# Kernel tuning notes

Hardware: AMD Instinct MI355X
Metric: run time of the kernel (lower is better)

## Reference

```python
import jax, jax.numpy as jnp
import numpy as np

DIM = 192; HEADS = 6; WS = 8; OVERLAP = 2; PAD = 3; STRIDE = WS - OVERLAP; HID = DIM * 4

_coords = np.stack(np.meshgrid(np.arange(WS), np.arange(WS), indexing='ij'), 0).reshape(2, -1)
_rel = (_coords[:, :, None] - _coords[:, None, :]).transpose(1, 2, 0).astype(np.int64)
_rel[..., 0] += WS - 1; _rel[..., 1] += WS - 1; _rel[..., 0] *= 2 * WS - 1
REL_IDX = jnp.asarray(_rel.sum(-1).reshape(-1))  # (WS^2 * WS^2,)


def _ln_c(x, g, b):
    # LayerNorm over channel dim of NCHW (LayerNormProxy)
    mu = jnp.mean(x, axis=1, keepdims=True)
    var = jnp.mean((x - mu) ** 2, axis=1, keepdims=True)
    return (x - mu) * jax.lax.rsqrt(var + 1e-5) * g[:, None, None] + b[:, None, None]


def _conv1x1(x, w, b):
    return jnp.einsum('bchw,oc->bohw', x, w) + b[:, None, None]


def _dwconv3(x, w, b):
    y = jax.lax.conv_general_dilated(x, w, (1, 1), ((1, 1), (1, 1)),
                                     feature_group_count=x.shape[1],
                                     dimension_numbers=('NCHW', 'OIHW', 'NCHW'))
    return y + b[:, None, None]


def _unfold(x, k, s, p):
    # F.unfold: (B,C,H,W) -> (B, C*k*k, L) with (C,kh,kw) channel order, row-major windows
    B, C, H, W = x.shape
    xp = jnp.pad(x, ((0, 0), (0, 0), (p, p), (p, p)))
    Lh = (H + 2 * p - k) // s + 1; Lw = (W + 2 * p - k) // s + 1
    ih = (jnp.arange(Lh) * s)[:, None] + jnp.arange(k)  # (Lh,k)
    iw = (jnp.arange(Lw) * s)[:, None] + jnp.arange(k)  # (Lw,k)
    t = xp[:, :, ih, :][:, :, :, :, iw]                 # (B,C,Lh,k,Lw,k)
    t = t.transpose(0, 1, 3, 5, 2, 4)                   # (B,C,k,k,Lh,Lw)
    return t.reshape(B, C * k * k, Lh * Lw)


def _fold(cols, h, w, k, s, p):
    # F.fold: (B, C*k*k, L) -> (B,C,h,w), summing overlaps
    B = cols.shape[0]
    Lh = (h + 2 * p - k) // s + 1; Lw = (w + 2 * p - k) // s + 1
    C = cols.shape[1] // (k * k)
    t = cols.reshape(B, C, k, k, Lh, Lw).transpose(0, 1, 4, 2, 5, 3)  # (B,C,Lh,k,Lw,k)
    ih = (jnp.arange(Lh) * s)[:, None] + jnp.arange(k)
    iw = (jnp.arange(Lw) * s)[:, None] + jnp.arange(k)
    out = jnp.zeros((B, C, h + 2 * p, w + 2 * p), cols.dtype)
    out = out.at[:, :, ih[:, :, None, None], iw[None, None, :, :]].add(t)
    return out[:, :, p:p + h, p:p + w]


def _reverse(win, h, w):
    B, L, nH, ws2, ch = win.shape
    cols = win.transpose(0, 2, 4, 3, 1).reshape(B, nH * ch * ws2, L)
    return _fold(cols, h, w, WS, STRIDE, PAD)


def _hft(x, w, b):
    # HFTAttention: high-frequency residual of multi-scale avg pools, dw-conv sigmoid gate
    B, C, h, ww = x.shape
    a = 3.0 * x
    for s in (2, 4, 8):
        pool = x.reshape(B, C, h // s, s, ww // s, s).mean(axis=(3, 5))
        a = a - jnp.repeat(jnp.repeat(pool, s, axis=2), s, axis=3)
    return jax.nn.sigmoid(_dwconv3(a, w, b)) * x


def _forward(x, n1g, n1b, qkv_w, qkv_b, temp, rpb, proj_w, proj_b, hft_w, hft_b,
             n2g, n2b, fc1_w, fc1_b, sgn_g, sgn_b, sg_w, sg_b, fc2_w, fc2_b):
    B, C, H, W = x.shape
    ch = C // HEADS
    y = _conv1x1(_ln_c(x, n1g, n1b), qkv_w, qkv_b)       # (B,3C,H,W)
    cols = _unfold(y, WS, STRIDE, PAD)
    L = cols.shape[-1]
    win = cols.reshape(B, 3 * HEADS, ch, WS * WS, L).transpose(0, 4, 1, 3, 2)  # (B,L,3H,ws2,ch)
    q = win[:, :, :HEADS] * temp[None, None]
    k = win[:, :, HEADS:2 * HEADS]
    v = win[:, :, 2 * HEADS:]
    attn = jnp.einsum('blhic,blhjc->blhij', q, k)
    bias = rpb[REL_IDX].reshape(WS * WS, WS * WS, HEADS).transpose(2, 0, 1)
    attn = attn + bias[None, None]
    e = jnp.exp(attn - jnp.max(attn, axis=-1, keepdims=True))
    s = jnp.sum(e, axis=-1, keepdims=True)               # (B,L,H,ws2,1)
    s_img = _reverse(s, H, W)                            # (B,HEADS,H,W): folded softmax denom
    o = jnp.einsum('blhij,blhjc->blhic', e, v)
    o_img = _reverse(o, H, W).reshape(B, HEADS, ch, H, W)
    out = (o_img / s_img[:, :, None]).reshape(B, C, H, W)
    out = _hft(_conv1x1(out, proj_w, proj_b), hft_w, hft_b)
    x1 = x + out
    z = jax.nn.gelu(_conv1x1(_ln_c(x1, n2g, n2b), fc1_w, fc1_b), approximate=False)
    z1, z2 = jnp.split(z, 2, axis=1)
    z = z1 * _dwconv3(_ln_c(z2, sgn_g, sgn_b), sg_w, sg_b)
    return x1 + _conv1x1(z, fc2_w, fc2_b)


def setup_inputs() -> dict:
    key = jax.random.key(0)
    ks = jax.random.split(key, 8)
    B, Hi, Wi = 4, 128, 128
    f = jnp.float32
    return {
        'x': jax.random.normal(ks[0], (B, DIM, Hi, Wi), f),
        'n1g': jnp.ones((DIM,), f), 'n1b': jnp.zeros((DIM,), f),
        'qkv_w': jax.random.normal(ks[1], (3 * DIM, DIM), f) * 0.02,
        'qkv_b': jnp.zeros((3 * DIM,), f),
        'temp': jnp.ones((HEADS, 1, 1), f),
        'rpb': jax.random.normal(ks[2], ((2 * WS - 1) ** 2, HEADS), f) * 0.02,
        'proj_w': jax.random.normal(ks[3], (DIM, DIM), f) * 0.02,
        'proj_b': jnp.zeros((DIM,), f),
        'hft_w': jax.random.normal(ks[4], (DIM, 1, 3, 3), f) * 0.02,
        'hft_b': jnp.zeros((DIM,), f),
        'n2g': jnp.ones((DIM,), f), 'n2b': jnp.zeros((DIM,), f),
        'fc1_w': jax.random.normal(ks[5], (HID, DIM), f) * 0.02,
        'fc1_b': jnp.zeros((HID,), f),
        'sgn_g': jnp.ones((HID // 2,), f), 'sgn_b': jnp.zeros((HID // 2,), f),
        'sg_w': jax.random.normal(ks[6], (HID // 2, 1, 3, 3), f) * 0.02,
        'sg_b': jnp.zeros((HID // 2,), f),
        'fc2_w': jax.random.normal(ks[7], (DIM, HID // 2), f) * 0.02,
        'fc2_b': jnp.zeros((DIM,), f),
    }


def reference(x, n1g, n1b, qkv_w, qkv_b, temp, rpb, proj_w, proj_b, hft_w, hft_b,
              n2g, n2b, fc1_w, fc1_b, sgn_g, sgn_b, sg_w, sg_b, fc2_w, fc2_b):
    return _forward(x, n1g, n1b, qkv_w, qkv_b, temp, rpb, proj_w, proj_b, hft_w, hft_b,
                    n2g, n2b, fc1_w, fc1_b, sgn_g, sgn_b, sg_w, sg_b, fc2_w, fc2_b)
```

## Files before the change

### kernel.cpp

```cpp
#include <hip/hip_runtime.h>
#include <math.h>

static constexpr int B_    = 4;
static constexpr int C_    = 192;
static constexpr int NPIX  = 16384;
static constexpr int PTOT  = B_ * NPIX;
static constexpr int HEADS = 6;
static constexpr int STR   = 6;
static constexpr int LH    = 22;
static constexpr int LWIN  = LH * LH;
static constexpr int NWIN  = B_ * LWIN;

typedef short bf16x8 __attribute__((ext_vector_type(8)));
typedef float f32x4  __attribute__((ext_vector_type(4)));

__device__ __forceinline__ unsigned short f2bf(float f) {
    union { float f; unsigned int u; } v; v.f = f;
    return (unsigned short)((v.u + 0x8000u) >> 16);
}
__device__ __forceinline__ float bf2f(unsigned short h) {
    union { unsigned int u; float f; } v; v.u = ((unsigned int)h) << 16;
    return v.f;
}
__device__ __forceinline__ float gelu_f(float v) {
    float u2 = 2.f * v * (0.7978845608f + 0.0356774081f * v * v);
    float e = __expf(u2);
    float th = 1.f - 2.f / (e + 1.f);
    return 0.5f * v * (1.f + th);
}

__global__ __launch_bounds__(256) void prep_k(const float* __restrict__ W, const float* __restrict__ g,
                                              const float* __restrict__ bln, const float* __restrict__ bias,
                                              int M, int K,
                                              unsigned short* __restrict__ wgb, float* __restrict__ wsum,
                                              float* __restrict__ wb) {
    int o = blockIdx.x * 256 + threadIdx.x;
    if (o >= M) return;
    float sum = 0.f, bb = 0.f;
    for (int c = 0; c < K; ++c) {
        float wv = W[(size_t)o * K + c];
        float wgv = wv * g[c];
        wgb[(size_t)o * K + c] = f2bf(wgv);
        sum += wgv;
        bb += wv * bln[c];
    }
    wsum[o] = sum;
    wb[o] = bb + bias[o];
}

__global__ __launch_bounds__(256) void wcvt_k(const float* __restrict__ W, unsigned short* __restrict__ Wb, int n) {
    int i = blockIdx.x * 256 + threadIdx.x;
    if (i < n) Wb[i] = f2bf(W[i]);
}

template <typename T, bool LNS>
__global__ __launch_bounds__(256) void transpose_k(const T* __restrict__ in, unsigned short* __restrict__ out,
                                                   int Cn, int bstride, float2* __restrict__ ps) {
    __shared__ float tile[64][65];
    int n0 = blockIdx.x << 6, c0 = blockIdx.y << 6, b = blockIdx.z;
    int t = threadIdx.x, r = t >> 2, cg = (t & 3) << 4;
    const T* ib = in + (size_t)b * bstride;
    if constexpr (sizeof(T) == 4) {
        const float4* src = (const float4*)(ib + (size_t)(c0 + r) * NPIX + n0 + cg);
        #pragma unroll
        for (int j = 0; j < 4; ++j) {
            float4 v = src[j];
            tile[r][cg + 4 * j + 0] = v.x; tile[r][cg + 4 * j + 1] = v.y;
            tile[r][cg + 4 * j + 2] = v.z; tile[r][cg + 4 * j + 3] = v.w;
        }
    } else {
        const uint4* src = (const uint4*)((const unsigned short*)ib + (size_t)(c0 + r) * NPIX + n0 + cg);
        uint4 v0 = src[0], v1 = src[1];
        unsigned int arr[8] = {v0.x, v0.y, v0.z, v0.w, v1.x, v1.y, v1.z, v1.w};
        #pragma unroll
        for (int j = 0; j < 8; ++j) {
            tile[r][cg + 2 * j]     = bf2f((unsigned short)(arr[j] & 0xFFFFu));
            tile[r][cg + 2 * j + 1] = bf2f((unsigned short)(arr[j] >> 16));
        }
    }
    __syncthreads();
    unsigned int pk[8];
    float s = 0.f, s2 = 0.f;
    #pragma unroll
    for (int j = 0; j < 8; ++j) {
        float a  = tile[cg + 2 * j][r];
        float c2 = tile[cg + 2 * j + 1][r];
        if (LNS) { s += a + c2; s2 += a * a + c2 * c2; }
        pk[j] = (unsigned int)f2bf(a) | ((unsigned int)f2bf(c2) << 16);
    }
    uint4* dst = (uint4*)(out + ((size_t)(b << 14) + n0 + r) * Cn + c0 + cg);
    dst[0] = make_uint4(pk[0], pk[1], pk[2], pk[3]);
    dst[1] = make_uint4(pk[4], pk[5], pk[6], pk[7]);
    if (LNS) {
        s  += __shfl_xor(s, 1);  s  += __shfl_xor(s, 2);
        s2 += __shfl_xor(s2, 1); s2 += __shfl_xor(s2, 2);
        if ((t & 3) == 0)
            ps[((b * gridDim.y + blockIdx.y) << 14) + n0 + r] = make_float2(s, s2);
    }
}

__global__ __launch_bounds__(256) void lnfin_k(const float2* __restrict__ ps, int nch, float invC,
                                               float* __restrict__ mu, float* __restrict__ rs) {
    int p = blockIdx.x * 256 + threadIdx.x;
    int b = p >> 14, n = p & (NPIX - 1);
    float s = 0.f, s2 = 0.f;
    for (int c = 0; c < nch; ++c) {
        float2 v = ps[((b * nch + c) << 14) + n];
        s += v.x; s2 += v.y;
    }
    float m = s * invC;
    mu[p] = m;
    rs[p] = rsqrtf(s2 * invC - m * m + 1e-5f);
}

template <int KK, int ACT, bool LN, bool RES, bool OBF, int STATS>
__global__ __launch_bounds__(256) void gemm2_k(const unsigned short* __restrict__ Wb,
                                               const unsigned short* __restrict__ Xt,
                                               void* __restrict__ outv,
                                               const float* __restrict__ mu, const float* __restrict__ rs,
                                               const float* __restrict__ wsum, const float* __restrict__ wb,
                                               const float* __restrict__ resid, int M,
                                               float* __restrict__ smu, float* __restrict__ srs) {
    constexpr int LDK    = KK + 8;
    constexpr int KSTEPS = KK / 32;
    __shared__ unsigned short xs[64 * LDK];

    int t = threadIdx.x;
    int pt = blockIdx.x;
    int b  = pt >> 8;
    int n0 = (pt & 255) << 6;

    const unsigned short* xg = Xt + (size_t)(b * NPIX + n0) * KK;
    constexpr int NJ = KK / 8;
    #pragma unroll
    for (int i = 0; i < 64 * NJ / 256; ++i) {
        int c = i * 256 + t;
        int p, j;
        if (KK == 192) { p = (c * 2731) >> 16; j = c - p * 24; }
        else           { int q = c >> 4; p = (q * 21846) >> 16; j = c - p * 48; }
        uint4 v = *(const uint4*)(xg + (size_t)c * 8);
        *(uint4*)&xs[p * LDK + j * 8] = v;
    }
    __syncthreads();

    int w  = t >> 6, l = t & 63;
    int wr = w >> 1, wc = w & 1;
    int lr = l & 15, kb = l >> 4;
    int pw = wr * 32;

    bf16x8 afr[KSTEPS][2];
    #pragma unroll
    for (int ks = 0; ks < KSTEPS; ++ks)
        #pragma unroll
        for (int m = 0; m < 2; ++m)
            afr[ks][m] = *(const bf16x8*)&xs[(pw + m * 16 + lr) * LDK + ks * 32 + kb * 8];

    float muv[2][4], rsv[2][4], murs[2][4];
    if (LN) {
        #pragma unroll
        for (int m = 0; m < 2; ++m) {
            int nidx = n0 + pw + m * 16 + kb * 4;
            #pragma unroll
            for (int r = 0; r < 4; ++r) {
                muv[m][r] = mu[(b << 14) + nidx + r];
                rsv[m][r] = rs[(b << 14) + nidx + r];
                murs[m][r] = muv[m][r] * rsv[m][r];
            }
        }
    }

    float zs[2][4], zs2[2][4];
    bool dstats = STATS && (blockIdx.y == gridDim.y - 1);
    if (STATS) {
        #pragma unroll
        for (int m = 0; m < 2; ++m)
            #pragma unroll
            for (int r = 0; r < 4; ++r) { zs[m][r] = 0.f; zs2[m][r] = 0.f; }
    }

    int mpb = (M >> 6) / gridDim.y;
    int ocbase = blockIdx.y * mpb;
    #pragma unroll 2
    for (int oc = 0; oc < mpb; ++oc) {
        int ow = ((ocbase + oc) << 6) + wc * 32;
        f32x4 acc[2][2];
        #pragma unroll
        for (int m = 0; m < 2; ++m)
            #pragma unroll
            for (int n = 0; n < 2; ++n) acc[m][n] = (f32x4){0.f, 0.f, 0.f, 0.f};

        #pragma unroll
        for (int ks = 0; ks < KSTEPS; ++ks) {
            bf16x8 bfr[2];
            #pragma unroll
            for (int n = 0; n < 2; ++n)
                bfr[n] = *(const bf16x8*)(Wb + (size_t)(ow + n * 16 + lr) * KK + ks * 32 + kb * 8);
            #pragma unroll
            for (int m = 0; m < 2; ++m)
                #pragma unroll
                for (int n = 0; n < 2; ++n)
                    acc[m][n] = __builtin_amdgcn_mfma_f32_16x16x32_bf16(afr[ks][m], bfr[n], acc[m][n], 0, 0, 0);
        }

        #pragma unroll
        for (int m = 0; m < 2; ++m) {
            int nidx = n0 + pw + m * 16 + kb * 4;
            #pragma unroll
            for (int n = 0; n < 2; ++n) {
                int o = ow + n * 16 + lr;
                float wbv = wb[o];
                float wsv = 0.f; if (LN) wsv = wsum[o];
                size_t obase = (((size_t)b * M + o) << 14) + nidx;
                float rv[4] = {0.f, 0.f, 0.f, 0.f};
                if (RES) {
                    float4 rr = *(const float4*)(resid + obase);
                    rv[0] = rr.x; rv[1] = rr.y; rv[2] = rr.z; rv[3] = rr.w;
                }
                float vo[4];
                #pragma unroll
                for (int r = 0; r < 4; ++r) {
                    float a = acc[m][n][r];
                    float v;
                    if (LN) { float t1 = fmaf(-murs[m][r], wsv, wbv); v = fmaf(rsv[m][r], a, t1); }
                    else    v = a + wbv;
                    if (ACT == 1) v = gelu_f(v);
                    vo[r] = v + rv[r];
                    if (STATS) {
                        if (dstats) { zs[m][r] += vo[r]; zs2[m][r] += vo[r] * vo[r]; }
                    }
                }
                if (OBF) {
                    ushort4 u;
                    u.x = f2bf(vo[0]); u.y = f2bf(vo[1]); u.z = f2bf(vo[2]); u.w = f2bf(vo[3]);
                    *(ushort4*)((unsigned short*)outv + obase) = u;
                } else {
                    float4 f = {vo[0], vo[1], vo[2], vo[3]};
                    *(float4*)((float*)outv + obase) = f;
                }
            }
        }
    }

    if (STATS) {
        if (dstats) {
            __shared__ float sst[64][2][2];
            #pragma unroll
            for (int m = 0; m < 2; ++m)
                #pragma unroll
                for (int r = 0; r < 4; ++r) {
                    float a  = zs[m][r], c2 = zs2[m][r];
                    a  += __shfl_xor(a, 1);  a  += __shfl_xor(a, 2);  a  += __shfl_xor(a, 4);  a  += __shfl_xor(a, 8);
                    c2 += __shfl_xor(c2, 1); c2 += __shfl_xor(c2, 2); c2 += __shfl_xor(c2, 4); c2 += __shfl_xor(c2, 8);
                    if (lr == 0) {
                        int pp = pw + m * 16 + kb * 4 + r;
                        sst[pp][wc][0] = a; sst[pp][wc][1] = c2;
                    }
                }
            __syncthreads();
            if (t < 64) {
                float ss  = sst[t][0][0] + sst[t][1][0];
                float ss2 = sst[t][0][1] + sst[t][1][1];
                float invC = 1.f / (float)(mpb << 6);
                float mm = ss * invC;
                smu[(b << 14) + n0 + t] = mm;
                srs[(b << 14) + n0 + t] = rsqrtf(ss2 * invC - mm * mm + 1e-5f);
            }
        }
    }
}

__global__ __launch_bounds__(64) void attn_mfma_k(const unsigned short* __restrict__ qkv,
                                                  const float* __restrict__ rpb,
                                                  const float* __restrict__ temp,
                                                  unsigned short* __restrict__ o_win,
                                                  float* __restrict__ s_win) {
    __shared__ unsigned short p_lds[64 * 72];
    __shared__ float rp[225];
    int wh = blockIdx.x;
    int head = wh % HEADS;
    int bw = wh / HEADS;
    int b = bw / LWIN, l = bw % LWIN;
    int sh = l / LH, sw = l % LH;
    int h0 = sh * STR - 3, w0 = sw * STR - 3;
    int t = threadIdx.x;
    int lr = t & 15, kb = t >> 4;

    for (int i = t; i < 225; i += 64) rp[i] = rpb[i * HEADS + head];
    float tmp = temp[head];

    const size_t qbase = ((size_t)(b * 576 + head * 32)) << 14;
    const unsigned short* qp = qkv + qbase;
    const unsigned short* kp = qkv + qbase + ((size_t)192 << 14);
    const unsigned short* vp = qkv + qbase + ((size_t)384 << 14);

    bf16x8 kf[4], qf[4];
    #pragma unroll
    for (int m = 0; m < 4; ++m) {
        int jp = m * 16 + lr;
        int hh = h0 + (jp >> 3), ww = w0 + (jp & 7);
        bool ok = ((unsigned)hh < 128u) && ((unsigned)ww < 128u);
        int pix = (hh << 7) + ww;
        #pragma unroll
        for (int j = 0; j < 8; ++j) {
            unsigned short kv = 0, qv = 0;
            if (ok) {
                size_t off = ((size_t)(kb * 8 + j) << 14) + pix;
                kv = kp[off];
                qv = qp[off];
            }
            kf[m][j] = (short)kv;
            qf[m][j] = (short)qv;
        }
    }

    f32x4 st[4][4];
    #pragma unroll
    for (int m = 0; m < 4; ++m)
        #pragma unroll
        for (int n = 0; n < 4; ++n) st[m][n] = (f32x4){0.f, 0.f, 0.f, 0.f};
    #pragma unroll
    for (int m = 0; m < 4; ++m)
        #pragma unroll
        for (int n = 0; n < 4; ++n)
            st[m][n] = __builtin_amdgcn_mfma_f32_16x16x32_bf16(kf[m], qf[n], st[m][n], 0, 0, 0);

    bf16x8 vf[2][2];
    #pragma unroll
    for (int np = 0; np < 2; ++np) {
        #pragma unroll
        for (int ks = 0; ks < 2; ++ks) {
            int hh = h0 + ks * 4 + kb;
            bool okr = (unsigned)hh < 128u;
            const unsigned short* vrow = vp + (((size_t)(np * 16 + lr)) << 14) + (hh << 7) + w0;
            #pragma unroll
            for (int j = 0; j < 8; ++j) {
                int ww = w0 + j;
                unsigned short vv = 0;
                if (okr && (unsigned)ww < 128u) vv = vrow[j];
                vf[np][ks][j] = (short)vv;
            }
        }
    }

    __syncthreads();

    #pragma unroll
    for (int n = 0; n < 4; ++n) {
        int i = n * 16 + lr;
        int iyy = i >> 3, ixx = i & 7;
        #pragma unroll
        for (int m = 0; m < 4; ++m) {
            #pragma unroll
            for (int r = 0; r < 4; ++r) {
                int j = m * 16 + kb * 4 + r;
                int dy = iyy - (j >> 3) + 7;
                int dx = ixx - (j & 7) + 7;
                st[m][n][r] = st[m][n][r] * tmp + rp[dy * 15 + dx];
            }
        }
    }

    #pragma unroll
    for (int n = 0; n < 4; ++n) {
        float mx = -1e30f;
        #pragma unroll
        for (int m = 0; m < 4; ++m)
            #pragma unroll
            for (int r = 0; r < 4; ++r) mx = fmaxf(mx, st[m][n][r]);
        mx = fmaxf(mx, __shfl_xor(mx, 16));
        mx = fmaxf(mx, __shfl_xor(mx, 32));
        float s = 0.f;
        #pragma unroll
        for (int m = 0; m < 4; ++m) {
            #pragma unroll
            for (int r = 0; r < 4; ++r) {
                float e = __expf(st[m][n][r] - mx);
                st[m][n][r] = e;
                s += e;
            }
        }
        s += __shfl_xor(s, 16);
        s += __shfl_xor(s, 32);
        int i = n * 16 + lr;
        if (kb == 0) s_win[(size_t)wh * 64 + i] = s;
        #pragma unroll
        for (int m = 0; m < 4; ++m) {
            unsigned int lo = (unsigned int)f2bf(st[m][n][0]) | ((unsigned int)f2bf(st[m][n][1]) << 16);
            unsigned int hi = (unsigned int)f2bf(st[m][n][2]) | ((unsigned int)f2bf(st[m][n][3]) << 16);
            *(unsigned int*)&p_lds[i * 72 + m * 16 + kb * 4]     = lo;
            *(unsigned int*)&p_lds[i * 72 + m * 16 + kb * 4 + 2] = hi;
        }
    }

    __syncthreads();

    f32x4 oc[4][2];
    #pragma unroll
    for (int m = 0; m < 4; ++m)
        #pragma unroll
        for (int np = 0; np < 2; ++np) oc[m][np] = (f32x4){0.f, 0.f, 0.f, 0.f};
    #pragma unroll
    for (int ks = 0; ks < 2; ++ks) {
        bf16x8 pa[4];
        #pragma unroll
        for (int m = 0; m < 4; ++m)
            pa[m] = *(const bf16x8*)&p_lds[(m * 16 + lr) * 72 + ks * 32 + kb * 8];
        #pragma unroll
        for (int m = 0; m < 4; ++m)
            #pragma unroll
            for (int np = 0; np < 2; ++np)
                oc[m][np] = __builtin_amdgcn_mfma_f32_16x16x32_bf16(pa[m], vf[np][ks], oc[m][np], 0, 0, 0);
    }

    unsigned short* ob = o_win + (size_t)wh * 2048;
    #pragma unroll
    for (int m = 0; m < 4; ++m) {
        int ibase = m * 16 + kb * 4;
        #pragma unroll
        for (int np = 0; np < 2; ++np) {
            int c = np * 16 + lr;
            #pragma unroll
            for (int r = 0; r < 4; ++r)
                ob[(ibase + r) * 32 + c] = f2bf(oc[m][np][r]);
        }
    }
}

__device__ __forceinline__ void win_range(int h, int& s0, int& s1) {
    s0 = (h + 1) / 6; if (s0 < 0) s0 = 0;
    s1 = (h + 3) / 6; if (s1 > 21) s1 = 21;
}

__global__ __launch_bounds__(256) void simg_k(const float* __restrict__ s_win, float* __restrict__ s_img) {
    int tid = blockIdx.x * 256 + threadIdx.x;
    if (tid >= B_ * HEADS * NPIX) return;
    int n = tid & (NPIX - 1);
    int bh = tid >> 14;
    int hd = bh % HEADS, b = bh / HEADS;
    int hy = n >> 7, wx = n & 127;
    int sy0, sy1, sx0, sx1;
    win_range(hy, sy0, sy1);
    win_range(wx, sx0, sx1);
    float acc = 0.f;
    for (int sy = sy0; sy <= sy1; ++sy)
        for (int sx = sx0; sx <= sx1; ++sx) {
            int idx = (hy - (sy * 6 - 3)) * 8 + (wx - (sx * 6 - 3));
            acc += s_win[(size_t)((b * LWIN + sy * LH + sx) * HEADS + hd) * 64 + idx];
        }
    s_img[tid] = acc;
}

__global__ __launch_bounds__(256) void fold_k(const unsigned short* __restrict__ o_win,
                                              const float* __restrict__ s_img,
                                              unsigned short* __restrict__ attn_t) {
    int tid = blockIdx.x * 256 + threadIdx.x;
    int q = (int)((((unsigned long long)(tid >> 3)) * 174763ull) >> 19);
    int oct = tid - q * 24;
    int n = q & (NPIX - 1), b = q >> 14;
    int hd = oct >> 2, c8 = (oct & 3) << 3;
    int hy = n >> 7, wx = n & 127;
    int sy0, sy1, sx0, sx1;
    win_range(hy, sy0, sy1);
    win_range(wx, sx0, sx1);
    float acc[8] = {0.f, 0.f, 0.f, 0.f, 0.f, 0.f, 0.f, 0.f};
    for (int sy = sy0; sy <= sy1; ++sy)
        for (int sx = sx0; sx <= sx1; ++sx) {
            int idx = (hy - (sy * 6 - 3)) * 8 + (wx - (sx * 6 - 3));
            const unsigned short* p = o_win + ((size_t)((b * LWIN + sy * LH + sx) * HEADS + hd) * 2048 + idx * 32 + c8);
            uint4 v = *(const uint4*)p;
            unsigned int arr[4] = {v.x, v.y, v.z, v.w};
            #pragma unroll
            for (int j = 0; j < 4; ++j) {
                acc[2 * j]     += bf2f((unsigned short)(arr[j] & 0xFFFFu));
                acc[2 * j + 1] += bf2f((unsigned short)(arr[j] >> 16));
            }
        }
    float inv = 1.f / s_img[((b * HEADS + hd) << 14) + n];
    unsigned int pk[4];
    #pragma unroll
    for (int j = 0; j < 4; ++j) {
        unsigned int lo = f2bf(acc[2 * j] * inv);
        unsigned int hi = f2bf(acc[2 * j + 1] * inv);
        pk[j] = lo | (hi << 16);
    }
    *(uint4*)&attn_t[((size_t)((b << 14) + n)) * 192 + hd * 32 + c8] = make_uint4(pk[0], pk[1], pk[2], pk[3]);
}

__global__ __launch_bounds__(256) void halve_k(const float* __restrict__ in, float* __restrict__ out, int Win) {
    int Wo = Win >> 1;
    int tot = B_ * C_ * Wo * Wo;
    int tid = blockIdx.x * 256 + threadIdx.x;
    if (tid >= tot) return;
    int xy = tid % (Wo * Wo);
    int bc = tid / (Wo * Wo);
    int y = xy / Wo, x = xy % Wo;
    const float* p = in + (size_t)bc * Win * Win + (size_t)(2 * y) * Win + 2 * x;
    out[tid] = 0.25f * (p[0] + p[1] + p[Win] + p[Win + 1]);
}

__global__ __launch_bounds__(256) void hft_fused_k(const float* __restrict__ po, const float* __restrict__ x,
                                                   const float* __restrict__ p2, const float* __restrict__ p4,
                                                   const float* __restrict__ p8, const float* __restrict__ hw,
                                                   const float* __restrict__ hb, float* __restrict__ x1) {
    __shared__ float tile[34 * 133];
    int rt = blockIdx.x, ch = blockIdx.y, b = blockIdx.z;
    int bc = b * C_ + ch;
    int y0 = rt << 5;
    int t = threadIdx.x;
    const float* pob = po + ((size_t)bc << 14);
    const float* p2b = p2 + ((size_t)bc << 12);
    const float* p4b = p4 + ((size_t)bc << 10);
    const float* p8b = p8 + ((size_t)bc << 8);

    for (int idx = t; idx < 34 * 133; idx += 256) {
        int row = idx / 133, col = idx - row * 133;
        int yy = y0 + row - 1, xw = col - 1;
        float val = 0.f;
        if (col < 130 && (unsigned)yy < 128u && (unsigned)xw < 128u) {
            int nn = (yy << 7) + xw;
            val = 3.f * pob[nn]
                - p2b[((yy >> 1) << 6) + (xw >> 1)]
                - p4b[((yy >> 2) << 5) + (xw >> 2)]
                - p8b[((yy >> 3) << 4) + (xw >> 3)];
        }
        tile[idx] = val;
    }
    __syncthreads();

    float wv[9];
    #pragma unroll
    for (int k = 0; k < 9; ++k) wv[k] = hw[ch * 9 + k];
    float hbv = hb[ch];

    int r = t & 31, c0 = (t >> 5) << 4;
    int nbase = ((y0 + r) << 7) + c0;
    const float* xb = x + ((size_t)bc << 14);
    float* x1b = x1 + ((size_t)bc << 14);

    float pov[16], xv[16];
    #pragma unroll
    for (int j4 = 0; j4 < 4; ++j4) {
        float4 pp = *(const float4*)(pob + nbase + 4 * j4);
        float4 xx = *(const float4*)(xb + nbase + 4 * j4);
        pov[4*j4] = pp.x; pov[4*j4+1] = pp.y; pov[4*j4+2] = pp.z; pov[4*j4+3] = pp.w;
        xv[4*j4] = xx.x;  xv[4*j4+1] = xx.y;  xv[4*j4+2] = xx.z;  xv[4*j4+3] = xx.w;
    }
    float res[16];
    #pragma unroll
    for (int j = 0; j < 16; ++j) {
        float acc = hbv;
        #pragma unroll
        for (int dy = 0; dy < 3; ++dy)
            #pragma unroll
            for (int dx = 0; dx < 3; ++dx)
                acc += wv[dy * 3 + dx] * tile[(r + dy) * 133 + c0 + j + dx];
        float sg = 1.f / (1.f + __expf(-acc));
        res[j] = xv[j] + sg * pov[j];
    }
    #pragma unroll
    for (int j4 = 0; j4 < 4; ++j4) {
        float4 o = {res[4*j4], res[4*j4+1], res[4*j4+2], res[4*j4+3]};
        *(float4*)(x1b + nbase + 4 * j4) = o;
    }
}

__global__ __launch_bounds__(256) void sgmul_k(unsigned short* __restrict__ z,
                                               const float* __restrict__ mu3, const float* __restrict__ rs3,
                                               const float* __restrict__ sgn_g, const float* __restrict__ sgn_b,
                                               const float* __restrict__ sg_w, const float* __restrict__ sg_b) {
    __shared__ float tile[34 * 133];
    int rt = blockIdx.x, ch = blockIdx.y, b = blockIdx.z;
    int y0 = rt << 5;
    int t = threadIdx.x;
    const unsigned short* zb = z + ((size_t)(b * 768 + 384 + ch) << 14);
    unsigned short* z1p = z + ((size_t)(b * 768 + ch) << 14);
    const float* mub = mu3 + (b << 14);
    const float* rsb = rs3 + (b << 14);
    float g = sgn_g[ch], bb = sgn_b[ch];

    for (int idx = t; idx < 34 * 133; idx += 256) {
        int row = idx / 133, col = idx - row * 133;
        int yy = y0 + row - 1, xw = col - 1;
        float val = 0.f;
        if (col < 130 && (unsigned)yy < 128u && (unsigned)xw < 128u) {
            int nn = (yy << 7) + xw;
            val = (bf2f(zb[nn]) - mub[nn]) * rsb[nn] * g + bb;
        }
        tile[idx] = val;
    }
    __syncthreads();

    float wv[9];
    #pragma unroll
    for (int k = 0; k < 9; ++k) wv[k] = sg_w[ch * 9 + k];
    float sb = sg_b[ch];

    int r = t & 31, c0 = (t >> 5) << 4;
    int nbase = ((y0 + r) << 7) + c0;

    float res[16];
    #pragma unroll
    for (int j = 0; j < 16; ++j) {
        float acc = sb;
        #pragma unroll
        for (int dy = 0; dy < 3; ++dy)
            #pragma unroll
            for (int dx = 0; dx < 3; ++dx)
                acc += wv[dy * 3 + dx] * tile[(r + dy) * 133 + c0 + j + dx];
        res[j] = acc;
    }
    uint4* zp = (uint4*)(z1p + nbase);
    uint4 v0 = zp[0], v1 = zp[1];
    unsigned int arr[8] = {v0.x, v0.y, v0.z, v0.w, v1.x, v1.y, v1.z, v1.w};
    #pragma unroll
    for (int j = 0; j < 8; ++j) {
        float lo = bf2f((unsigned short)(arr[j] & 0xFFFFu)) * res[2 * j];
        float hi = bf2f((unsigned short)(arr[j] >> 16)) * res[2 * j + 1];
        arr[j] = (unsigned int)f2bf(lo) | ((unsigned int)f2bf(hi) << 16);
    }
    zp[0] = make_uint4(arr[0], arr[1], arr[2], arr[3]);
    zp[1] = make_uint4(arr[4], arr[5], arr[6], arr[7]);
}

extern "C" void kernel_launch(void* const* d_in, const int* in_sizes, int n_in,
                              void* d_out, int out_size, void* d_ws, size_t ws_size,
                              hipStream_t stream) {
    const float* x     = (const float*)d_in[0];
    const float* n1g   = (const float*)d_in[1];
    const float* n1b   = (const float*)d_in[2];
    const float* qkv_w = (const float*)d_in[3];
    const float* qkv_b = (const float*)d_in[4];
    const float* temp  = (const float*)d_in[5];
    const float* rpb   = (const float*)d_in[6];
    const float* proj_w= (const float*)d_in[7];
    const float* proj_b= (const float*)d_in[8];
    const float* hft_w = (const float*)d_in[9];
    const float* hft_b = (const float*)d_in[10];
    const float* n2g   = (const float*)d_in[11];
    const float* n2b   = (const float*)d_in[12];
    const float* fc1_w = (const float*)d_in[13];
    const float* fc1_b = (const float*)d_in[14];
    const float* sgn_g = (const float*)d_in[15];
    const float* sgn_b = (const float*)d_in[16];
    const float* sg_w  = (const float*)d_in[17];
    const float* sg_b  = (const float*)d_in[18];
    const float* fc2_w = (const float*)d_in[19];
    const float* fc2_b = (const float*)d_in[20];
    float* out = (float*)d_out;
    float* w = (float*)d_ws;

    float* mu1 = w;            float* rs1 = w + 65536;
    float* mu2 = w + 131072;   float* rs2 = w + 196608;
    float* mu3 = w + 262144;   float* rs3 = w + 327680;
    unsigned short* wgb_qkv = (unsigned short*)(w + 393216);
    float* wsum_qkv = w + 448512;  float* wb_qkv = w + 449088;
    unsigned short* wgb_fc1 = (unsigned short*)(w + 449664);
    float* wsum_fc1 = w + 523392;  float* wb_fc1 = w + 524160;
    unsigned short* pwb  = (unsigned short*)(w + 524928);
    unsigned short* f2wb = (unsigned short*)(w + 543360);
    unsigned short* xt     = (unsigned short*)(w + 580224);
    unsigned short* attn_t = xt;
    unsigned short* qkvb = (unsigned short*)(w + 6871680);
    float* proj_out = w + 6871680;
    float* p2 = w + 19454592;  float* p4 = w + 22600320;  float* p8 = w + 23386752;
    unsigned short* x1t  = (unsigned short*)(w + 6871680);
    unsigned short* z1t  = (unsigned short*)(w + 6871680);
    unsigned short* o_win = (unsigned short*)(w + 25746048);
    float* s_win = w + 49535616;
    float* s_img = w + 50279040;
    unsigned short* z = (unsigned short*)(w + 25746048);
    float* x1 = w + 50911872;
    float2* ps = (float2*)(w + 19454592);

    transpose_k<float, true><<<dim3(256, 3, B_), 256, 0, stream>>>(x, xt, 192, 192 * NPIX, ps);
    lnfin_k<<<256, 256, 0, stream>>>(ps, 3, 1.f / 192.f, mu1, rs1);
    prep_k<<<3, 256, 0, stream>>>(qkv_w, n1g, n1b, qkv_b, 576, 192, wgb_qkv, wsum_qkv, wb_qkv);
    gemm2_k<192, 0, true, false, true, 0><<<dim3(1024, 3), 256, 0, stream>>>(
        wgb_qkv, xt, qkvb, mu1, rs1, wsum_qkv, wb_qkv, nullptr, 576, nullptr, nullptr);
    attn_mfma_k<<<NWIN * HEADS, 64, 0, stream>>>(qkvb, rpb, temp, o_win, s_win);
    simg_k<<<1536, 256, 0, stream>>>(s_win, s_img);
    fold_k<<<6144, 256, 0, stream>>>(o_win, s_img, attn_t);
    wcvt_k<<<144, 256, 0, stream>>>(proj_w, pwb, 192 * 192);
    gemm2_k<192, 0, false, false, false, 0><<<dim3(1024, 3), 256, 0, stream>>>(
        pwb, attn_t, proj_out, nullptr, nullptr, nullptr, proj_b, nullptr, 192, nullptr, nullptr);
    halve_k<<<12288, 256, 0, stream>>>(proj_out, p2, 128);
    halve_k<<<3072, 256, 0, stream>>>(p2, p4, 64);
    halve_k<<<768, 256, 0, stream>>>(p4, p8, 32);
    hft_fused_k<<<dim3(4, 192, B_), 256, 0, stream>>>(proj_out, x, p2, p4, p8, hft_w, hft_b, x1);
    transpose_k<float, true><<<dim3(256, 3, B_), 256, 0, stream>>>(x1, x1t, 192, 192 * NPIX, ps);
    lnfin_k<<<256, 256, 0, stream>>>(ps, 3, 1.f / 192.f, mu2, rs2);
    prep_k<<<3, 256, 0, stream>>>(fc1_w, n2g, n2b, fc1_b, 768, 192, wgb_fc1, wsum_fc1, wb_fc1);
    gemm2_k<192, 1, true, false, true, 1><<<dim3(1024, 2), 256, 0, stream>>>(
        wgb_fc1, x1t, z, mu2, rs2, wsum_fc1, wb_fc1, nullptr, 768, mu3, rs3);
    sgmul_k<<<dim3(4, 384, B_), 256, 0, stream>>>(z, mu3, rs3, sgn_g, sgn_b, sg_w, sg_b);
    transpose_k<unsigned short, false><<<dim3(256, 6, B_), 256, 0, stream>>>(z, z1t, 384, 768 * NPIX, nullptr);
    wcvt_k<<<288, 256, 0, stream>>>(fc2_w, f2wb, 192 * 384);
    gemm2_k<384, 0, false, true, false, 0><<<dim3(1024, 1), 256, 0, stream>>>(
        f2wb, z1t, out, nullptr, nullptr, nullptr, fc2_b, x1, 192, nullptr, nullptr);
}
```

Measured before the change: 648.3 us.

## Retile GEMM grids, store proj output in bf16, split LN stats, use fast packing

The GEMM kernel now takes its per-block output-chunk count as a template constant, and the grids are retuned: fc1 runs over 4 column groups and fc2 over 3 instead of 1, which gives more blocks for parallelism. The fused LN statistics for the second half of z move out of the fc1 GEMM into a separate reduction kernel, and the proj output is written as bf16 rather than fp32, cutting traffic into the halve and hft kernels. Conversions use a perm-based bf16 pack, reciprocals use rcp, and GELU gets a cheaper formula. The costs are an extra pass over z, lower precision on the proj output, and more fc2 blocks each reloading the activation tile.

Result: slower. 690.8 us (+6.6%).

```diff
diff --git a/kernel.cpp b/kernel.cpp
--- a/kernel.cpp
+++ b/kernel.cpp
@@ -22,11 +22,16 @@
     union { unsigned int u; float f; } v; v.u = ((unsigned int)h) << 16;
     return v.f;
 }
+__device__ __forceinline__ unsigned int pack2bf(float a, float b) {
+    union { float f; unsigned int u; } x, y; x.f = a; y.f = b;
+    return __builtin_amdgcn_perm(y.u + 0x8000u, x.u + 0x8000u, 0x07060302u);
+}
 __device__ __forceinline__ float gelu_f(float v) {
-    float u2 = 2.f * v * (0.7978845608f + 0.0356774081f * v * v);
-    float e = __expf(u2);
-    float th = 1.f - 2.f / (e + 1.f);
-    return 0.5f * v * (1.f + th);
+    float vv = v * v;
+    float u  = v * fmaf(vv, 0.0713548162f, 1.5957691216f);
+    float e  = __expf(u);
+    float r  = __builtin_amdgcn_rcpf(e + 1.f);
+    return (u > 80.f) ? v : v * e * r;
 }
 
 __global__ __launch_bounds__(256) void prep_k(const float* __restrict__ W, const float* __restrict__ g,
@@ -86,7 +91,7 @@
         float a  = tile[cg + 2 * j][r];
         float c2 = tile[cg + 2 * j + 1][r];
         if (LNS) { s += a + c2; s2 += a * a + c2 * c2; }
-        pk[j] = (unsigned int)f2bf(a) | ((unsigned int)f2bf(c2) << 16);
+        pk[j] = pack2bf(a, c2);
     }
     uint4* dst = (uint4*)(out + ((size_t)(b << 14) + n0 + r) * Cn + c0 + cg);
     dst[0] = make_uint4(pk[0], pk[1], pk[2], pk[3]);
@@ -113,14 +118,36 @@
     rs[p] = rsqrtf(s2 * invC - m * m + 1e-5f);
 }
 
-template <int KK, int ACT, bool LN, bool RES, bool OBF, int STATS>
+__global__ __launch_bounds__(256) void lnstats_z2_k(const unsigned short* __restrict__ z,
+                                                    float* __restrict__ mu, float* __restrict__ rs) {
+    __shared__ float red[2][4][64];
+    int n0 = blockIdx.x << 6, b = blockIdx.y;
+    int t = threadIdx.x;
+    int px = n0 + (t & 63), cg = t >> 6;
+    float s = 0.f, s2 = 0.f;
+    for (int c = cg; c < 384; c += 4) {
+        float v = bf2f(z[((size_t)(b * 768 + 384 + c) << 14) + px]);
+        s += v; s2 += v * v;
+    }
+    red[0][cg][t & 63] = s;
+    red[1][cg][t & 63] = s2;
+    __syncthreads();
+    if (t < 64) {
+        float ss  = red[0][0][t] + red[0][1][t] + red[0][2][t] + red[0][3][t];
+        float ss2 = red[1][0][t] + red[1][1][t] + red[1][2][t] + red[1][3][t];
+        float m = ss * (1.f / 384.f);
+        mu[(b << 14) + n0 + t] = m;
+        rs[(b << 14) + n0 + t] = rsqrtf(ss2 * (1.f / 384.f) - m * m + 1e-5f);
+    }
+}
+
+template <int KK, int MPB, int ACT, bool LN, bool RES, bool OBF>
 __global__ __launch_bounds__(256) void gemm2_k(const unsigned short* __restrict__ Wb,
                                                const unsigned short* __restrict__ Xt,
                                                void* __restrict__ outv,
                                                const float* __restrict__ mu, const float* __restrict__ rs,
                                                const float* __restrict__ wsum, const float* __restrict__ wb,
-                                               const float* __restrict__ resid, int M,
-                                               float* __restrict__ smu, float* __restrict__ srs) {
+                                               const float* __restrict__ resid, int M) {
     constexpr int LDK    = KK + 8;
     constexpr int KSTEPS = KK / 32;
     __shared__ unsigned short xs[64 * LDK];
@@ -155,33 +182,23 @@
         for (int m = 0; m < 2; ++m)
             afr[ks][m] = *(const bf16x8*)&xs[(pw + m * 16 + lr) * LDK + ks * 32 + kb * 8];
 
-    float muv[2][4], rsv[2][4], murs[2][4];
+    float rsv[2][4], murs[2][4];
     if (LN) {
         #pragma unroll
         for (int m = 0; m < 2; ++m) {
             int nidx = n0 + pw + m * 16 + kb * 4;
             #pragma unroll
             for (int r = 0; r < 4; ++r) {
-                muv[m][r] = mu[(b << 14) + nidx + r];
+                float mv = mu[(b << 14) + nidx + r];
                 rsv[m][r] = rs[(b << 14) + nidx + r];
-                murs[m][r] = muv[m][r] * rsv[m][r];
+                murs[m][r] = mv * rsv[m][r];
             }
         }
     }
 
-    float zs[2][4], zs2[2][4];
-    bool dstats = STATS && (blockIdx.y == gridDim.y - 1);
-    if (STATS) {
-        #pragma unroll
-        for (int m = 0; m < 2; ++m)
-            #pragma unroll
-            for (int r = 0; r < 4; ++r) { zs[m][r] = 0.f; zs2[m][r] = 0.f; }
-    }
-
-    int mpb = (M >> 6) / gridDim.y;
-    int ocbase = blockIdx.y * mpb;
-    #pragma unroll 2
-    for (int oc = 0; oc < mpb; ++oc) {
+    int ocbase = blockIdx.y * MPB;
+    #pragma unroll
+    for (int oc = 0; oc < MPB; ++oc) {
         int ow = ((ocbase + oc) << 6) + wc * 32;
         f32x4 acc[2][2];
         #pragma unroll
@@ -225,45 +242,16 @@
                     else    v = a + wbv;
                     if (ACT == 1) v = gelu_f(v);
                     vo[r] = v + rv[r];
-                    if (STATS) {
-                        if (dstats) { zs[m][r] += vo[r]; zs2[m][r] += vo[r] * vo[r]; }
-                    }
                 }
                 if (OBF) {
-                    ushort4 u;
-                    u.x = f2bf(vo[0]); u.y = f2bf(vo[1]); u.z = f2bf(vo[2]); u.w = f2bf(vo[3]);
-                    *(ushort4*)((unsigned short*)outv + obase) = u;
+                    uint2 u;
+                    u.x = pack2bf(vo[0], vo[1]);
+                    u.y = pack2bf(vo[2], vo[3]);
+                    *(uint2*)((unsigned short*)outv + obase) = u;
                 } else {
                     float4 f = {vo[0], vo[1], vo[2], vo[3]};
                     *(float4*)((float*)outv + obase) = f;
                 }
-            }
-        }
-    }
-
-    if (STATS) {
-        if (dstats) {
-            __shared__ float sst[64][2][2];
-            #pragma unroll
-            for (int m = 0; m < 2; ++m)
-                #pragma unroll
-                for (int r = 0; r < 4; ++r) {
-                    float a  = zs[m][r], c2 = zs2[m][r];
-                    a  += __shfl_xor(a, 1);  a  += __shfl_xor(a, 2);  a  += __shfl_xor(a, 4);  a  += __shfl_xor(a, 8);
-                    c2 += __shfl_xor(c2, 1); c2 += __shfl_xor(c2, 2); c2 += __shfl_xor(c2, 4); c2 += __shfl_xor(c2, 8);
-                    if (lr == 0) {
-                        int pp = pw + m * 16 + kb * 4 + r;
-                        sst[pp][wc][0] = a; sst[pp][wc][1] = c2;
-                    }
-                }
-            __syncthreads();
-            if (t < 64) {
-                float ss  = sst[t][0][0] + sst[t][1][0];
-                float ss2 = sst[t][0][1] + sst[t][1][1];
-                float invC = 1.f / (float)(mpb << 6);
-                float mm = ss * invC;
-                smu[(b << 14) + n0 + t] = mm;
-                srs[(b << 14) + n0 + t] = rsqrtf(ss2 * invC - mm * mm + 1e-5f);
             }
         }
     }
@@ -385,10 +373,8 @@
         if (kb == 0) s_win[(size_t)wh * 64 + i] = s;
         #pragma unroll
         for (int m = 0; m < 4; ++m) {
-            unsigned int lo = (unsigned int)f2bf(st[m][n][0]) | ((unsigned int)f2bf(st[m][n][1]) << 16);
-            unsigned int hi = (unsigned int)f2bf(st[m][n][2]) | ((unsigned int)f2bf(st[m][n][3]) << 16);
-            *(unsigned int*)&p_lds[i * 72 + m * 16 + kb * 4]     = lo;
-            *(unsigned int*)&p_lds[i * 72 + m * 16 + kb * 4 + 2] = hi;
+            *(unsigned int*)&p_lds[i * 72 + m * 16 + kb * 4]     = pack2bf(st[m][n][0], st[m][n][1]);
+            *(unsigned int*)&p_lds[i * 72 + m * 16 + kb * 4 + 2] = pack2bf(st[m][n][2], st[m][n][3]);
         }
     }
 
@@ -475,18 +461,16 @@
                 acc[2 * j + 1] += bf2f((unsigned short)(arr[j] >> 16));
             }
         }
-    float inv = 1.f / s_img[((b * HEADS + hd) << 14) + n];
+    float inv = __builtin_amdgcn_rcpf(s_img[((b * HEADS + hd) << 14) + n]);
     unsigned int pk[4];
     #pragma unroll
-    for (int j = 0; j < 4; ++j) {
-        unsigned int lo = f2bf(acc[2 * j] * inv);
-        unsigned int hi = f2bf(acc[2 * j + 1] * inv);
-        pk[j] = lo | (hi << 16);
-    }
+    for (int j = 0; j < 4; ++j)
+        pk[j] = pack2bf(acc[2 * j] * inv, acc[2 * j + 1] * inv);
     *(uint4*)&attn_t[((size_t)((b << 14) + n)) * 192 + hd * 32 + c8] = make_uint4(pk[0], pk[1], pk[2], pk[3]);
 }
 
-__global__ __launch_bounds__(256) void halve_k(const float* __restrict__ in, float* __restrict__ out, int Win) {
+template <typename TI>
+__global__ __launch_bounds__(256) void halve_k(const TI* __restrict__ in, float* __restrict__ out, int Win) {
     int Wo = Win >> 1;
     int tot = B_ * C_ * Wo * Wo;
     int tid = blockIdx.x * 256 + threadIdx.x;
@@ -494,11 +478,17 @@
     int xy = tid % (Wo * Wo);
     int bc = tid / (Wo * Wo);
     int y = xy / Wo, x = xy % Wo;
-    const float* p = in + (size_t)bc * Win * Win + (size_t)(2 * y) * Win + 2 * x;
-    out[tid] = 0.25f * (p[0] + p[1] + p[Win] + p[Win + 1]);
-}
-
-__global__ __launch_bounds__(256) void hft_fused_k(const float* __restrict__ po, const float* __restrict__ x,
+    const TI* p = in + (size_t)bc * Win * Win + (size_t)(2 * y) * Win + 2 * x;
+    float a, bq, c, d;
+    if constexpr (sizeof(TI) == 2) {
+        a = bf2f(p[0]); bq = bf2f(p[1]); c = bf2f(p[Win]); d = bf2f(p[Win + 1]);
+    } else {
+        a = p[0]; bq = p[1]; c = p[Win]; d = p[Win + 1];
+    }
+    out[tid] = 0.25f * (a + bq + c + d);
+}
+
+__global__ __launch_bounds__(256) void hft_fused_k(const unsigned short* __restrict__ po, const float* __restrict__ x,
                                                    const float* __restrict__ p2, const float* __restrict__ p4,
                                                    const float* __restrict__ p8, const float* __restrict__ hw,
                                                    const float* __restrict__ hb, float* __restrict__ x1) {
@@ -507,7 +497,7 @@
     int bc = b * C_ + ch;
     int y0 = rt << 5;
     int t = threadIdx.x;
-    const float* pob = po + ((size_t)bc << 14);
+    const unsigned short* pob = po + ((size_t)bc << 14);
     const float* p2b = p2 + ((size_t)bc << 12);
     const float* p4b = p4 + ((size_t)bc << 10);
     const float* p8b = p8 + ((size_t)bc << 8);
@@ -518,7 +508,7 @@
         float val = 0.f;
         if (col < 130 && (unsigned)yy < 128u && (unsigned)xw < 128u) {
             int nn = (yy << 7) + xw;
-            val = 3.f * pob[nn]
+            val = 3.f * bf2f(pob[nn])
                 - p2b[((yy >> 1) << 6) + (xw >> 1)]
                 - p4b[((yy >> 2) << 5) + (xw >> 2)]
                 - p8b[((yy >> 3) << 4) + (xw >> 3)];
@@ -538,12 +528,20 @@
     float* x1b = x1 + ((size_t)bc << 14);
 
     float pov[16], xv[16];
-    #pragma unroll
-    for (int j4 = 0; j4 < 4; ++j4) {
-        float4 pp = *(const float4*)(pob + nbase + 4 * j4);
-        float4 xx = *(const float4*)(xb + nbase + 4 * j4);
-        pov[4*j4] = pp.x; pov[4*j4+1] = pp.y; pov[4*j4+2] = pp.z; pov[4*j4+3] = pp.w;
-        xv[4*j4] = xx.x;  xv[4*j4+1] = xx.y;  xv[4*j4+2] = xx.z;  xv[4*j4+3] = xx.w;
+    {
+        const uint4* pp4 = (const uint4*)(pob + nbase);
+        uint4 a0 = pp4[0], a1 = pp4[1];
+        unsigned int arr[8] = {a0.x, a0.y, a0.z, a0.w, a1.x, a1.y, a1.z, a1.w};
+        #pragma unroll
+        for (int j = 0; j < 8; ++j) {
+            pov[2 * j]     = bf2f((unsigned short)(arr[j] & 0xFFFFu));
+            pov[2 * j + 1] = bf2f((unsigned short)(arr[j] >> 16));
+        }
+        #pragma unroll
+        for (int j4 = 0; j4 < 4; ++j4) {
+            float4 xx = *(const float4*)(xb + nbase + 4 * j4);
+            xv[4*j4] = xx.x; xv[4*j4+1] = xx.y; xv[4*j4+2] = xx.z; xv[4*j4+3] = xx.w;
+        }
     }
     float res[16];
     #pragma unroll
@@ -554,7 +552,7 @@
             #pragma unroll
             for (int dx = 0; dx < 3; ++dx)
                 acc += wv[dy * 3 + dx] * tile[(r + dy) * 133 + c0 + j + dx];
-        float sg = 1.f / (1.f + __expf(-acc));
+        float sg = __builtin_amdgcn_rcpf(1.f + __expf(-acc));
         res[j] = xv[j] + sg * pov[j];
     }
     #pragma unroll
@@ -616,7 +614,7 @@
     for (int j = 0; j < 8; ++j) {
         float lo = bf2f((unsigned short)(arr[j] & 0xFFFFu)) * res[2 * j];
         float hi = bf2f((unsigned short)(arr[j] >> 16)) * res[2 * j + 1];
-        arr[j] = (unsigned int)f2bf(lo) | ((unsigned int)f2bf(hi) << 16);
+        arr[j] = pack2bf(lo, hi);
     }
     zp[0] = make_uint4(arr[0], arr[1], arr[2], arr[3]);
     zp[1] = make_uint4(arr[4], arr[5], arr[6], arr[7]);
@@ -661,7 +659,7 @@
     unsigned short* xt     = (unsigned short*)(w + 580224);
     unsigned short* attn_t = xt;
     unsigned short* qkvb = (unsigned short*)(w + 6871680);
-    float* proj_out = w + 6871680;
+    unsigned short* proj_out = (unsigned short*)(w + 6871680);
     float* p2 = w + 19454592;  float* p4 = w + 22600320;  float* p8 = w + 23386752;
     unsigned short* x1t  = (unsigned short*)(w + 6871680);
     unsigned short* z1t  = (unsigned short*)(w + 6871680);
@@ -675,26 +673,27 @@
     transpose_k<float, true><<<dim3(256, 3, B_), 256, 0, stream>>>(x, xt, 192, 192 * NPIX, ps);
     lnfin_k<<<256, 256, 0, stream>>>(ps, 3, 1.f / 192.f, mu1, rs1);
     prep_k<<<3, 256, 0, stream>>>(qkv_w, n1g, n1b, qkv_b, 576, 192, wgb_qkv, wsum_qkv, wb_qkv);
-    gemm2_k<192, 0, true, false, true, 0><<<dim3(1024, 3), 256, 0, stream>>>(
-        wgb_qkv, xt, qkvb, mu1, rs1, wsum_qkv, wb_qkv, nullptr, 576, nullptr, nullptr);
+    gemm2_k<192, 3, 0, true, false, true><<<dim3(1024, 3), 256, 0, stream>>>(
+        wgb_qkv, xt, qkvb, mu1, rs1, wsum_qkv, wb_qkv, nullptr, 576);
     attn_mfma_k<<<NWIN * HEADS, 64, 0, stream>>>(qkvb, rpb, temp, o_win, s_win);
     simg_k<<<1536, 256, 0, stream>>>(s_win, s_img);
     fold_k<<<6144, 256, 0, stream>>>(o_win, s_img, attn_t);
     wcvt_k<<<144, 256, 0, stream>>>(proj_w, pwb, 192 * 192);
-    gemm2_k<192, 0, false, false, false, 0><<<dim3(1024, 3), 256, 0, stream>>>(
-        pwb, attn_t, proj_out, nullptr, nullptr, nullptr, proj_b, nullptr, 192, nullptr, nullptr);
-    halve_k<<<12288, 256, 0, stream>>>(proj_out, p2, 128);
-    halve_k<<<3072, 256, 0, stream>>>(p2, p4, 64);
-    halve_k<<<768, 256, 0, stream>>>(p4, p8, 32);
+    gemm2_k<192, 1, 0, false, false, true><<<dim3(1024, 3), 256, 0, stream>>>(
+        pwb, attn_t, proj_out, nullptr, nullptr, nullptr, proj_b, nullptr, 192);
+    halve_k<unsigned short><<<12288, 256, 0, stream>>>(proj_out, p2, 128);
+    halve_k<float><<<3072, 256, 0, stream>>>(p2, p4, 64);
+    halve_k<float><<<768, 256, 0, stream>>>(p4, p8, 32);
     hft_fused_k<<<dim3(4, 192, B_), 256, 0, stream>>>(proj_out, x, p2, p4, p8, hft_w, hft_b, x1);
     transpose_k<float, true><<<dim3(256, 3, B_), 256, 0, stream>>>(x1, x1t, 192, 192 * NPIX, ps);
     lnfin_k<<<256, 256, 0, stream>>>(ps, 3, 1.f / 192.f, mu2, rs2);
     prep_k<<<3, 256, 0, stream>>>(fc1_w, n2g, n2b, fc1_b, 768, 192, wgb_fc1, wsum_fc1, wb_fc1);
-    gemm2_k<192, 1, true, false, true, 1><<<dim3(1024, 2), 256, 0, stream>>>(
-        wgb_fc1, x1t, z, mu2, rs2, wsum_fc1, wb_fc1, nullptr, 768, mu3, rs3);
+    gemm2_k<192, 3, 1, true, false, true><<<dim3(1024, 4), 256, 0, stream>>>(
+        wgb_fc1, x1t, z, mu2, rs2, wsum_fc1, wb_fc1, nullptr, 768);
+    lnstats_z2_k<<<dim3(256, B_), 256, 0, stream>>>(z, mu3, rs3);
     sgmul_k<<<dim3(4, 384, B_), 256, 0, stream>>>(z, mu3, rs3, sgn_g, sgn_b, sg_w, sg_b);
     transpose_k<unsigned short, false><<<dim3(256, 6, B_), 256, 0, stream>>>(z, z1t, 384, 768 * NPIX, nullptr);
     wcvt_k<<<288, 256, 0, stream>>>(fc2_w, f2wb, 192 * 384);
-    gemm2_k<384, 0, false, true, false, 0><<<dim3(1024, 1), 256, 0, stream>>>(
-        f2wb, z1t, out, nullptr, nullptr, nullptr, fc2_b, x1, 192, nullptr, nullptr);
-}
+    gemm2_k<384, 1, 0, false, true, false><<<dim3(1024, 3), 256, 0, stream>>>(
+        f2wb, z1t, out, nullptr, nullptr, nullptr, fc2_b, x1, 192);
+}
```
